# Performance work log

Measured on AMD Instinct MI355X. Metric: run time of the kernel, lower is better.

Reference implementation:

```python
import jax, jax.numpy as jnp
import numpy as np

D = 300   # hidden dim (Linear(300,300))
L = 160   # seq len, forced by W3 = Linear(160,1)


def _linear(x, W, b):
    # torch Linear: x @ W.T + b, W is (out, in)
    return jnp.matmul(x, W.T) + b


def setup_inputs() -> dict:
    key = jax.random.key(0)
    ks = jax.random.split(key, 16)
    B = 1024
    s = 1.0 / np.sqrt(D)
    inp = {
        'T_feature': jax.random.normal(ks[0], (B, L, D), jnp.float32),
        'CD_feature': jax.random.normal(ks[1], (B, L, D), jnp.float32),
        'Wproj': jax.random.normal(ks[2], (D, D), jnp.float32) * s,
        'bproj': jnp.zeros((D,), jnp.float32),
        'WqT_w': jax.random.normal(ks[3], (D, D), jnp.float32) * s,
        'WqT_b': jnp.zeros((D,), jnp.float32),
        'WqCD_w': jax.random.normal(ks[4], (D, D), jnp.float32) * s,
        'WqCD_b': jnp.zeros((D,), jnp.float32),
        'WkT_w': jax.random.normal(ks[5], (D, D), jnp.float32) * s,
        'WkT_b': jnp.zeros((D,), jnp.float32),
        'WkCD_w': jax.random.normal(ks[6], (D, D), jnp.float32) * s,
        'WkCD_b': jnp.zeros((D,), jnp.float32),
        'W3_w': jax.random.normal(ks[7], (1, L), jnp.float32) * (1.0 / np.sqrt(L)),
        'W3_b': jnp.zeros((1,), jnp.float32),
    }
    return inp


def reference(T_feature, CD_feature, Wproj, bproj, WqT_w, WqT_b, WqCD_w, WqCD_b,
              WkT_w, WkT_b, WkCD_w, WkCD_b, W3_w, W3_b):
    sqrt_d = jnp.sqrt(jnp.float32(D))
    proj_T = _linear(T_feature, Wproj, bproj)     # (B, L, D)
    proj_CD = _linear(CD_feature, Wproj, bproj)   # (B, L, D)

    # N_tensor @ proj_T is just the mean over tokens (weights 1/Len)
    mean_T = jnp.mean(proj_T, axis=1, keepdims=True)          # (B, 1, D)
    qT = _linear(mean_T, WqT_w, WqT_b)                        # (B, 1, D)
    kT = _linear(proj_T, WkT_w, WkT_b)                        # (B, L, D)
    alphaT = jnp.einsum('bqd,bkd->bqk', qT, kT) / sqrt_d      # (B, 1, L)
    ZT = jax.nn.sigmoid(alphaT)

    qCD = _linear(proj_CD, WqCD_w, WqCD_b)                    # (B, L, D)
    kCD = _linear(proj_CD, WkCD_w, WkCD_b)                    # (B, L, D)
    alphaCD = jnp.einsum('bqd,bkd->bqk', qCD, kCD) / sqrt_d   # (B, L, L)
    ZCD = jax.nn.sigmoid(alphaCD)

    # The per-token loop+cat is a plain broadcast multiply: Mt[:,i,:] = ZCD[:,i,:] * ZT[:,0,:]
    Mt = ZCD * ZT                                             # (B, L, L)
    alpha_f = jax.nn.softmax(_linear(Mt, W3_w, W3_b), axis=1) # (B, L, 1)

    # Second loop is a per-token scalar scale: HCD[:,i,:] = alpha_f[:,i,0] * proj_CD[:,i,:]
    HCD = alpha_f * proj_CD                                   # (B, L, D)
    return (proj_T, HCD)
```

## Files before the change

kernel.cpp:

```cpp
#include <hip/hip_runtime.h>
#include <hip/hip_bf16.h>


typedef __attribute__((ext_vector_type(8))) short short8;
typedef __attribute__((ext_vector_type(4))) float f32x4;

#define DP 320

__device__ __forceinline__ unsigned short f2bf(float x) {
  unsigned int u = __builtin_bit_cast(unsigned int, x);
  u += 0x7FFFu + ((u >> 16) & 1u);
  return (unsigned short)(u >> 16);
}
__device__ __forceinline__ float bf2f(unsigned short h) {
  unsigned int u = ((unsigned int)h) << 16;
  return __builtin_bit_cast(float, u);
}
__device__ __forceinline__ void gload16(const void* g, void* l) {
  __builtin_amdgcn_global_load_lds(
      (const __attribute__((address_space(1))) unsigned int*)g,
      (__attribute__((address_space(3))) unsigned int*)l, 16, 0, 0);
}
__device__ __forceinline__ float sigm(float x) { return 1.0f / (1.0f + __expf(-x)); }
__device__ __forceinline__ int swzc(int r, int c) {
  return (c & ~63) | ((((c >> 3) & 7) ^ (r & 7)) << 3) | (c & 7);
}

__global__ void wb_k(const float* __restrict__ W, unsigned short* __restrict__ Wb) {
  int n = blockIdx.x, c = threadIdx.x;
  unsigned short v = (n < 300 && c < 300) ? f2bf(W[n * 300 + c]) : (unsigned short)0;
  Wb[n * DP + swzc(n, c)] = v;
}

__global__ void crossdot_k(const float* __restrict__ Wa, const float* __restrict__ ba,
                           const float* __restrict__ Wc, const float* __restrict__ bc,
                           unsigned short* __restrict__ out_h, float* __restrict__ out_f,
                           float scale) {
  int n = blockIdx.x, c = threadIdx.x;
  float v = 0.f;
  if (n <= 300 && c <= 300) {
    for (int o = 0; o < 300; ++o) {
      float a = (c < 300) ? Wa[o * 300 + c] : ba[o];
      float b = (n < 300) ? Wc[o * 300 + n] : bc[o];
      v += a * b;
    }
    v *= scale;
  }
  if (out_h) out_h[n * DP + swzc(n, c)] = f2bf(v);
  else       out_f[n * DP + c] = v;
}

__global__ __launch_bounds__(256)
void cvt_k(const float* __restrict__ T, const float* __restrict__ CD,
           unsigned short* __restrict__ Abf) {
  unsigned idx = blockIdx.x * 256 + threadIdx.x;
  if (idx >= 327680u * 40u) return;
  unsigned row = idx / 40u, G = idx - row * 40u;
  int kc = G >> 3, sg = G & 7;
  int col0 = kc * 64 + (sg ^ ((int)row & 7)) * 8;
  const float* base = (row < 163840u) ? T + (size_t)row * 300
                                      : CD + (size_t)(row - 163840u) * 300;
  short8 h;
  if (col0 + 8 <= 300) {
    f32x4 x0 = *(const f32x4*)(base + col0), x1 = *(const f32x4*)(base + col0 + 4);
#pragma unroll
    for (int j = 0; j < 4; ++j) { h[j] = (short)f2bf(x0[j]); h[j + 4] = (short)f2bf(x1[j]); }
  } else {
#pragma unroll
    for (int j = 0; j < 8; ++j) {
      int c = col0 + j;
      h[j] = (short)((c < 300) ? f2bf(base[c]) : (unsigned short)0);
    }
  }
  *(short8*)(Abf + (size_t)row * DP + G * 8) = h;
}

__global__ __launch_bounds__(512)
void gemm_k(const unsigned short* __restrict__ Abf, const unsigned short* __restrict__ pCDg,
            const unsigned short* __restrict__ Wb, const unsigned short* __restrict__ Maug,
            const float* __restrict__ bias, float* __restrict__ Of,
            unsigned short* __restrict__ pCDout, unsigned short* __restrict__ Yout,
            int mode_base) {
  __shared__ __align__(16) unsigned short As[2][256 * 64];
  __shared__ __align__(16) unsigned short Bs[2][320 * 64];
  const int tid = threadIdx.x, wid = tid >> 6, lane = tid & 63;
  const int lr = lane & 15, hi = lane >> 4;
  const int mode = mode_base + blockIdx.y;
  const unsigned short* __restrict__ A =
      (mode == 0) ? Abf : (mode == 1) ? Abf + (size_t)163840 * DP : pCDg;
  const unsigned short* __restrict__ Bm = (mode == 2) ? Maug : Wb;
  const size_t m0 = (size_t)blockIdx.x * 256;

  f32x4 acc[4][10];
#pragma unroll
  for (int i = 0; i < 4; ++i)
#pragma unroll
    for (int j = 0; j < 10; ++j) acc[i][j] = (f32x4){0.f, 0.f, 0.f, 0.f};

  auto stageA = [&](int buf, int kc) {
#pragma unroll
    for (int it = 0; it < 4; ++it) {
      int idx = it * 512 + tid;
      int row = idx >> 3, g = idx & 7;
      gload16(A + (m0 + row) * DP + kc * 64 + g * 8, (char*)As[buf] + idx * 16);
    }
  };
  auto stageB = [&](int buf, int kc) {
#pragma unroll
    for (int it = 0; it < 5; ++it) {
      int idx = it * 512 + tid;
      int row = idx >> 3, g = idx & 7;
      gload16(Bm + (size_t)row * DP + kc * 64 + g * 8, (char*)Bs[buf] + idx * 16);
    }
  };

  stageA(0, 0); stageB(0, 0);
  __syncthreads();
  int buf = 0;
  const int rm = (wid >> 1) * 64, cn = (wid & 1) * 160;
  for (int kc = 0; kc < 5; ++kc) {
    if (kc < 4) { stageA(buf ^ 1, kc + 1); stageB(buf ^ 1, kc + 1); }
#pragma unroll
    for (int kk = 0; kk < 2; ++kk) {
      const int slot = ((kk * 4 + hi) ^ lr) & 7;
      short8 a[4];
#pragma unroll
      for (int mf = 0; mf < 4; ++mf)
        a[mf] = *(const short8*)((const char*)As[buf] + (rm + mf * 16 + lr) * 128 + slot * 16);
#pragma unroll
      for (int nh = 0; nh < 2; ++nh) {
        short8 b[5];
#pragma unroll
        for (int nf = 0; nf < 5; ++nf)
          b[nf] = *(const short8*)((const char*)Bs[buf] +
                                   (cn + (nh * 5 + nf) * 16 + lr) * 128 + slot * 16);
#pragma unroll
        for (int mf = 0; mf < 4; ++mf)
#pragma unroll
          for (int nf = 0; nf < 5; ++nf)
            acc[mf][nh * 5 + nf] =
                __builtin_amdgcn_mfma_f32_16x16x32_bf16(a[mf], b[nf], acc[mf][nh * 5 + nf], 0, 0, 0);
      }
    }
    __syncthreads();
    buf ^= 1;
  }

#pragma unroll
  for (int mf = 0; mf < 4; ++mf)
#pragma unroll
    for (int nf = 0; nf < 10; ++nf) {
      const int col = cn + nf * 16 + lr;
      const float bv = (mode < 2 && col < 300) ? bias[col] : 0.f;
#pragma unroll
      for (int r = 0; r < 4; ++r) {
        const size_t row = m0 + rm + mf * 16 + hi * 4 + r;
        float v = acc[mf][nf][r] + bv;
        if (mode == 0) {
          if (col < 300) Of[row * 300 + col] = v;
        } else {
          unsigned short u = (mode == 2) ? f2bf(v)
                           : (col < 300) ? f2bf(v)
                           : (col == 300) ? f2bf(1.0f) : (unsigned short)0;
          unsigned short* dst = (mode == 1) ? pCDout : Yout;
          dst[row * DP + swzc((int)row, col)] = u;
        }
      }
    }
}

__global__ __launch_bounds__(320)
void gate_k(const float* __restrict__ projT, const float* __restrict__ Pmat,
            float* __restrict__ ZT) {
  __shared__ float mt[304];
  __shared__ float vv[304];
  const int b = blockIdx.x, tid = threadIdx.x, wid = tid >> 6, lane = tid & 63;
  const float* p = projT + (size_t)b * 48000;
  if (tid < 300) {
    float s = 0.f;
#pragma unroll 4
    for (int l = 0; l < 160; ++l) s += p[l * 300 + tid];
    mt[tid] = s * (1.0f / 160.0f);
  }
  __syncthreads();
  if (tid <= 300) {
    float s = Pmat[300 * DP + tid];
    for (int a = 0; a < 300; ++a) s += Pmat[a * DP + tid] * mt[a];
    vv[tid] = s;
  }
  __syncthreads();
  for (int j = wid * 32; j < wid * 32 + 32; ++j) {
    const float* row = p + j * 300;
    float s = 0.f;
    for (int c = lane; c < 300; c += 64) s += vv[c] * row[c];
#pragma unroll
    for (int m = 1; m < 64; m <<= 1) s += __shfl_xor(s, m, 64);
    if (lane == 0) ZT[b * 160 + j] = sigm(s + vv[300]);
  }
}

__global__ __launch_bounds__(320)
void finale_k(const unsigned short* __restrict__ Yg, const unsigned short* __restrict__ Pg,
              const float* __restrict__ ZT, const float* __restrict__ W3w,
              float* __restrict__ out) {
  __shared__ __align__(16) unsigned short Ps[160 * DP];
  __shared__ __align__(16) unsigned short Ys[2][160 * 64];
  __shared__ float t_arr[160];
  __shared__ float s_arr[160];
  __shared__ float red0;
  const int b = blockIdx.x, tid = threadIdx.x, wid = tid >> 6, lane = tid & 63;
  const int lr = lane & 15, hi = lane >> 4;
  const unsigned short* Pb = Pg + (size_t)b * 160 * DP;
  const unsigned short* Yb = Yg + (size_t)b * 160 * DP;

  if (tid < 160) t_arr[tid] = ZT[b * 160 + tid] * W3w[tid];

#pragma unroll
  for (int it = 0; it < 20; ++it) {
    int idx = it * 320 + tid;
    gload16(Pb + (size_t)idx * 8, (char*)Ps + idx * 16);
  }
  auto stageY = [&](int buf, int kc) {
#pragma unroll
    for (int it = 0; it < 4; ++it) {
      int idx = it * 320 + tid;
      int row = idx >> 3, g = idx & 7;
      gload16(Yb + (size_t)row * DP + kc * 64 + g * 8, (char*)Ys[buf] + idx * 16);
    }
  };

  f32x4 acc[2][10];
#pragma unroll
  for (int i = 0; i < 2; ++i)
#pragma unroll
    for (int j = 0; j < 10; ++j) acc[i][j] = (f32x4){0.f, 0.f, 0.f, 0.f};

  stageY(0, 0);
  __syncthreads();
  int buf = 0;
  const int rm = wid * 32;
  for (int kc = 0; kc < 5; ++kc) {
    if (kc < 4) stageY(buf ^ 1, kc + 1);
#pragma unroll
    for (int kk = 0; kk < 2; ++kk) {
      const int slot = ((kk * 4 + hi) ^ lr) & 7;
      short8 a[2], bb[10];
#pragma unroll
      for (int mf = 0; mf < 2; ++mf)
        a[mf] = *(const short8*)((const char*)Ys[buf] + (rm + mf * 16 + lr) * 128 + slot * 16);
#pragma unroll
      for (int nf = 0; nf < 10; ++nf)
        bb[nf] = *(const short8*)((const char*)Ps + (nf * 16 + lr) * 640 + (kc * 8 + slot) * 16);
#pragma unroll
      for (int mf = 0; mf < 2; ++mf)
#pragma unroll
        for (int nf = 0; nf < 10; ++nf)
          acc[mf][nf] = __builtin_amdgcn_mfma_f32_16x16x32_bf16(a[mf], bb[nf], acc[mf][nf], 0, 0, 0);
    }
    __syncthreads();
    buf ^= 1;
  }

  float pp[2][4];
#pragma unroll
  for (int mf = 0; mf < 2; ++mf)
#pragma unroll
    for (int r = 0; r < 4; ++r) {
      float s = 0.f;
#pragma unroll
      for (int nf = 0; nf < 10; ++nf) s += sigm(acc[mf][nf][r]) * t_arr[nf * 16 + lr];
      pp[mf][r] = s;
    }
#pragma unroll
  for (int m = 1; m < 16; m <<= 1)
#pragma unroll
    for (int mf = 0; mf < 2; ++mf)
#pragma unroll
      for (int r = 0; r < 4; ++r) pp[mf][r] += __shfl_xor(pp[mf][r], m, 64);
  if (lr == 0) {
#pragma unroll
    for (int mf = 0; mf < 2; ++mf)
#pragma unroll
      for (int r = 0; r < 4; ++r)
        s_arr[rm + mf * 16 + hi * 4 + r] = pp[mf][r];
  }
  __syncthreads();
  if (wid == 0) {
    float v0 = s_arr[lane], v1 = s_arr[lane + 64];
    float v2 = (lane < 32) ? s_arr[lane + 128] : -3.0e38f;
    float mx = fmaxf(fmaxf(v0, v1), v2);
#pragma unroll
    for (int m = 1; m < 64; m <<= 1) mx = fmaxf(mx, __shfl_xor(mx, m, 64));
    float e0 = __expf(v0 - mx), e1 = __expf(v1 - mx);
    float e2 = (lane < 32) ? __expf(v2 - mx) : 0.f;
    s_arr[lane] = e0; s_arr[lane + 64] = e1;
    if (lane < 32) s_arr[lane + 128] = e2;
    float sm = e0 + e1 + e2;
#pragma unroll
    for (int m = 1; m < 64; m <<= 1) sm += __shfl_xor(sm, m, 64);
    if (lane == 0) red0 = 1.0f / sm;
  }
  __syncthreads();
  const float inv = red0;
  float* ob = out + (size_t)b * 48000;
#pragma unroll 2
  for (int it = 0; it < 19; ++it) {
    int idx = it * 320 + tid;
    if (idx < 6080) {
      int i = idx / 38, cg = idx - i * 38;
      int sg = (cg & ~7) | ((cg & 7) ^ (i & 7));
      short8 pv = *(const short8*)((const char*)Ps + i * 640 + sg * 16);
      float sc = s_arr[i] * inv;
      int c0 = cg * 8;
#pragma unroll
      for (int j = 0; j < 8; ++j) {
        int c = c0 + j;
        if (c < 300) ob[(size_t)i * 300 + c] = sc * bf2f((unsigned short)pv[j]);
      }
    }
  }
}

extern "C" void kernel_launch(void* const* d_in, const int* in_sizes, int n_in,
                              void* d_out, int out_size, void* d_ws, size_t ws_size,
                              hipStream_t stream) {
  (void)in_sizes; (void)n_in; (void)out_size; (void)ws_size;
  const float* T      = (const float*)d_in[0];
  const float* CD     = (const float*)d_in[1];
  const float* Wproj  = (const float*)d_in[2];
  const float* bproj  = (const float*)d_in[3];
  const float* WqT_w  = (const float*)d_in[4];
  const float* WqT_b  = (const float*)d_in[5];
  const float* WqCD_w = (const float*)d_in[6];
  const float* WqCD_b = (const float*)d_in[7];
  const float* WkT_w  = (const float*)d_in[8];
  const float* WkT_b  = (const float*)d_in[9];
  const float* WkCD_w = (const float*)d_in[10];
  const float* WkCD_b = (const float*)d_in[11];
  const float* W3_w   = (const float*)d_in[12];

  char* ws = (char*)d_ws;
  size_t off = 0;
  auto alloc = [&](size_t bytes) { void* p = ws + off; off = (off + bytes + 255) & ~(size_t)255; return p; };
  unsigned short* Abf   = (unsigned short*)alloc((size_t)327680 * DP * 2);
  unsigned short* Wb    = (unsigned short*)alloc((size_t)DP * DP * 2);
  unsigned short* MaugT = (unsigned short*)alloc((size_t)DP * DP * 2);
  float* Pmat = (float*)alloc((size_t)DP * DP * 4);
  float* ZT   = (float*)alloc((size_t)1024 * 160 * 4);

  float* projT = (float*)d_out;
  float* HCD   = (float*)d_out + (size_t)49152000;
  unsigned short* pCDg = Abf + (size_t)163840 * DP;
  unsigned short* Yg   = Abf;

  const float isd = 1.0f / sqrtf(300.0f);

  wb_k<<<dim3(320), dim3(320), 0, stream>>>(Wproj, Wb);
  crossdot_k<<<dim3(320), dim3(320), 0, stream>>>(WqCD_w, WqCD_b, WkCD_w, WkCD_b, MaugT, nullptr, isd);
  crossdot_k<<<dim3(320), dim3(320), 0, stream>>>(WkT_w, WkT_b, WqT_w, WqT_b, nullptr, Pmat, isd);
  cvt_k<<<dim3(51200), dim3(256), 0, stream>>>(T, CD, Abf);

  gemm_k<<<dim3(640, 2), dim3(512), 0, stream>>>(Abf, pCDg, Wb, MaugT, bproj,
                                                 projT, pCDg, Yg, 0);
  gate_k<<<dim3(1024), dim3(320), 0, stream>>>(projT, Pmat, ZT);
  gemm_k<<<dim3(640, 1), dim3(512), 0, stream>>>(Abf, pCDg, Wb, MaugT, bproj,
                                                 projT, pCDg, Yg, 2);
  finale_k<<<dim3(1024), dim3(320), 0, stream>>>(Yg, pCDg, ZT, W3_w, HCD);
}
```

Baseline: 775.5 us.

## Fold projection into attention weights so all three GEMMs run in one launch

Precomputes G = Maug·Wproj and a bias vector so the Y GEMM reads the raw bf16 CD input, not the projected pCD. This removes the dependency between the projection GEMM and the Y GEMM, so all three run as one gemm_k grid when the workspace is large enough for separate pCD and Y buffers. The gate kernel is rewritten to read the bf16 T input and fold Wproj into its vectors rather than reread the fp32 projT output. The cost is extra prep kernels and workspace, plus some accuracy risk because bf16 now feeds the gate path and the composed weight matrix is rounded to bf16.

```diff
diff --git a/kernel.cpp b/kernel.cpp
--- a/kernel.cpp
+++ b/kernel.cpp
@@ -26,28 +26,63 @@
   return (c & ~63) | ((((c >> 3) & 7) ^ (r & 7)) << 3) | (c & 7);
 }
 
-__global__ void wb_k(const float* __restrict__ W, unsigned short* __restrict__ Wb) {
-  int n = blockIdx.x, c = threadIdx.x;
-  unsigned short v = (n < 300 && c < 300) ? f2bf(W[n * 300 + c]) : (unsigned short)0;
-  Wb[n * DP + swzc(n, c)] = v;
-}
-
-__global__ void crossdot_k(const float* __restrict__ Wa, const float* __restrict__ ba,
-                           const float* __restrict__ Wc, const float* __restrict__ bc,
-                           unsigned short* __restrict__ out_h, float* __restrict__ out_f,
-                           float scale) {
-  int n = blockIdx.x, c = threadIdx.x;
+__global__ __launch_bounds__(320)
+void prep1_k(const float* __restrict__ W,
+             const float* __restrict__ WqCD_w, const float* __restrict__ WqCD_b,
+             const float* __restrict__ WkCD_w, const float* __restrict__ WkCD_b,
+             const float* __restrict__ WqT_w, const float* __restrict__ WqT_b,
+             const float* __restrict__ WkT_w, const float* __restrict__ WkT_b,
+             unsigned short* __restrict__ Wb, float* __restrict__ Wt,
+             unsigned short* __restrict__ MaugT, float* __restrict__ Maug_f,
+             float* __restrict__ Pmat, float isd) {
+  const int x = blockIdx.x, c = threadIdx.x;
+  if (x < 320) {
+    const int n = x;
+    unsigned short v = (n < 300 && c < 300) ? f2bf(W[n * 300 + c]) : (unsigned short)0;
+    Wb[n * DP + swzc(n, c)] = v;
+    if (n < 300 && c < 300) Wt[c * 304 + n] = W[n * 300 + c];
+  } else if (x < 640) {
+    const int n = x - 320;
+    float v = 0.f;
+    if (n <= 300 && c <= 300) {
+      for (int o = 0; o < 300; ++o) {
+        float a = (c < 300) ? WqCD_w[o * 300 + c] : WqCD_b[o];
+        float b = (n < 300) ? WkCD_w[o * 300 + n] : WkCD_b[o];
+        v += a * b;
+      }
+      v *= isd;
+    }
+    MaugT[n * DP + swzc(n, c)] = f2bf(v);
+    Maug_f[n * DP + c] = v;
+  } else {
+    const int n = x - 640;
+    float v = 0.f;
+    if (n <= 300 && c <= 300) {
+      for (int o = 0; o < 300; ++o) {
+        float a = (c < 300) ? WkT_w[o * 300 + c] : WkT_b[o];
+        float b = (n < 300) ? WqT_w[o * 300 + n] : WqT_b[o];
+        v += a * b;
+      }
+      v *= isd;
+    }
+    Pmat[n * DP + c] = v;
+  }
+}
+
+__global__ __launch_bounds__(320)
+void gh_k(const float* __restrict__ Maug_f, const float* __restrict__ W,
+          const float* __restrict__ bproj, unsigned short* __restrict__ Gswz,
+          float* __restrict__ h) {
+  const int n = blockIdx.x, o = threadIdx.x;
   float v = 0.f;
-  if (n <= 300 && c <= 300) {
-    for (int o = 0; o < 300; ++o) {
-      float a = (c < 300) ? Wa[o * 300 + c] : ba[o];
-      float b = (n < 300) ? Wc[o * 300 + n] : bc[o];
-      v += a * b;
-    }
-    v *= scale;
-  }
-  if (out_h) out_h[n * DP + swzc(n, c)] = f2bf(v);
-  else       out_f[n * DP + c] = v;
+  if (o < 300) {
+    for (int c = 0; c < 300; ++c) v += Maug_f[n * DP + c] * W[c * 300 + o];
+  } else if (o == 300) {
+    float s = 0.f;
+    for (int c = 0; c < 300; ++c) s += Maug_f[n * DP + c] * bproj[c];
+    h[n] = s + Maug_f[n * DP + 300];
+  }
+  Gswz[n * DP + swzc(n, o)] = (o < 300) ? f2bf(v) : (unsigned short)0;
 }
 
 __global__ __launch_bounds__(256)
@@ -57,7 +92,7 @@
   if (idx >= 327680u * 40u) return;
   unsigned row = idx / 40u, G = idx - row * 40u;
   int kc = G >> 3, sg = G & 7;
-  int col0 = kc * 64 + (sg ^ ((int)row & 7)) * 8;
+  int col0 = kc * 64 + ((sg ^ ((int)row & 7)) << 3);
   const float* base = (row < 163840u) ? T + (size_t)row * 300
                                       : CD + (size_t)(row - 163840u) * 300;
   short8 h;
@@ -76,19 +111,19 @@
 }
 
 __global__ __launch_bounds__(512)
-void gemm_k(const unsigned short* __restrict__ Abf, const unsigned short* __restrict__ pCDg,
-            const unsigned short* __restrict__ Wb, const unsigned short* __restrict__ Maug,
-            const float* __restrict__ bias, float* __restrict__ Of,
-            unsigned short* __restrict__ pCDout, unsigned short* __restrict__ Yout,
-            int mode_base) {
+void gemm_k(const unsigned short* __restrict__ A0, const unsigned short* __restrict__ A1,
+            const unsigned short* __restrict__ A2,
+            const unsigned short* __restrict__ B01, const unsigned short* __restrict__ B2,
+            const float* __restrict__ bias, const float* __restrict__ ybias,
+            float* __restrict__ Of, unsigned short* __restrict__ pCDout,
+            unsigned short* __restrict__ Yout, int mode_base) {
   __shared__ __align__(16) unsigned short As[2][256 * 64];
   __shared__ __align__(16) unsigned short Bs[2][320 * 64];
   const int tid = threadIdx.x, wid = tid >> 6, lane = tid & 63;
   const int lr = lane & 15, hi = lane >> 4;
   const int mode = mode_base + blockIdx.y;
-  const unsigned short* __restrict__ A =
-      (mode == 0) ? Abf : (mode == 1) ? Abf + (size_t)163840 * DP : pCDg;
-  const unsigned short* __restrict__ Bm = (mode == 2) ? Maug : Wb;
+  const unsigned short* __restrict__ A = (mode == 0) ? A0 : (mode == 1) ? A1 : A2;
+  const unsigned short* __restrict__ Bm = (mode == 2) ? B2 : B01;
   const size_t m0 = (size_t)blockIdx.x * 256;
 
   f32x4 acc[4][10];
@@ -151,7 +186,9 @@
 #pragma unroll
     for (int nf = 0; nf < 10; ++nf) {
       const int col = cn + nf * 16 + lr;
-      const float bv = (mode < 2 && col < 300) ? bias[col] : 0.f;
+      float bv;
+      if (mode == 2) bv = ybias ? ybias[col] : 0.f;
+      else bv = (col < 300) ? bias[col] : 0.f;
 #pragma unroll
       for (int r = 0; r < 4; ++r) {
         const size_t row = m0 + rm + mf * 16 + hi * 4 + r;
@@ -170,32 +207,78 @@
 }
 
 __global__ __launch_bounds__(320)
-void gate_k(const float* __restrict__ projT, const float* __restrict__ Pmat,
-            float* __restrict__ ZT) {
-  __shared__ float mt[304];
+void gate2_k(const unsigned short* __restrict__ AbfT, const float* __restrict__ Pmat,
+             const float* __restrict__ W, const float* __restrict__ Wt,
+             const float* __restrict__ bproj, float* __restrict__ ZT) {
+  __shared__ float part[8][320];
+  __shared__ float ml[320];
+  __shared__ float maug[304];
   __shared__ float vv[304];
-  const int b = blockIdx.x, tid = threadIdx.x, wid = tid >> 6, lane = tid & 63;
-  const float* p = projT + (size_t)b * 48000;
-  if (tid < 300) {
+  __shared__ float wt[320];
+  __shared__ float cpr;
+  const int b = blockIdx.x, t = threadIdx.x;
+  const int wid = t >> 6, lane = t & 63;
+  const size_t sbase = (size_t)b * 160 * DP;
+  {
+    const int og = t % 40, seg = t / 40;
+    float a8[8] = {0.f, 0.f, 0.f, 0.f, 0.f, 0.f, 0.f, 0.f};
+    for (int l = seg * 20; l < seg * 20 + 20; ++l) {
+      int sg = (og & ~7) | ((og & 7) ^ (l & 7));
+      short8 v = *(const short8*)(AbfT + sbase + (size_t)l * DP + sg * 8);
+#pragma unroll
+      for (int j = 0; j < 8; ++j) a8[j] += bf2f((unsigned short)v[j]);
+    }
+#pragma unroll
+    for (int j = 0; j < 8; ++j) part[seg][og * 8 + j] = a8[j];
+  }
+  __syncthreads();
+  {
     float s = 0.f;
-#pragma unroll 4
-    for (int l = 0; l < 160; ++l) s += p[l * 300 + tid];
-    mt[tid] = s * (1.0f / 160.0f);
-  }
-  __syncthreads();
-  if (tid <= 300) {
-    float s = Pmat[300 * DP + tid];
-    for (int a = 0; a < 300; ++a) s += Pmat[a * DP + tid] * mt[a];
-    vv[tid] = s;
+#pragma unroll
+    for (int sg = 0; sg < 8; ++sg) s += part[sg][t];
+    ml[t] = s * (1.0f / 160.0f);
+  }
+  __syncthreads();
+  if (t < 304) {
+    if (t < 300) {
+      float s = 0.f;
+      for (int o = 0; o < 300; ++o) s += Wt[o * 304 + t] * ml[o];
+      maug[t] = s + bproj[t];
+    } else maug[t] = (t == 300) ? 1.f : 0.f;
+  }
+  __syncthreads();
+  if (t < 304) {
+    float s = 0.f;
+    if (t <= 300) for (int a = 0; a <= 300; ++a) s += Pmat[a * DP + t] * maug[a];
+    vv[t] = s;
+  }
+  __syncthreads();
+  if (t < 320) {
+    if (t < 300) {
+      float s = 0.f;
+      for (int c = 0; c < 300; ++c) s += vv[c] * W[c * 300 + t];
+      wt[t] = s;
+    } else {
+      wt[t] = 0.f;
+      if (t == 300) {
+        float s = 0.f;
+        for (int c = 0; c < 300; ++c) s += vv[c] * bproj[c];
+        cpr = s + vv[300];
+      }
+    }
   }
   __syncthreads();
   for (int j = wid * 32; j < wid * 32 + 32; ++j) {
-    const float* row = p + j * 300;
     float s = 0.f;
-    for (int c = lane; c < 300; c += 64) s += vv[c] * row[c];
+    if (lane < 40) {
+      int sg = (lane & ~7) | ((lane & 7) ^ (j & 7));
+      short8 v = *(const short8*)(AbfT + sbase + (size_t)j * DP + sg * 8);
+#pragma unroll
+      for (int k = 0; k < 8; ++k) s += bf2f((unsigned short)v[k]) * wt[lane * 8 + k];
+    }
 #pragma unroll
     for (int m = 1; m < 64; m <<= 1) s += __shfl_xor(s, m, 64);
-    if (lane == 0) ZT[b * 160 + j] = sigm(s + vv[300]);
+    if (lane == 0) ZT[b * 160 + j] = sigm(s + cpr);
   }
 }
 
@@ -324,7 +407,7 @@
 extern "C" void kernel_launch(void* const* d_in, const int* in_sizes, int n_in,
                               void* d_out, int out_size, void* d_ws, size_t ws_size,
                               hipStream_t stream) {
-  (void)in_sizes; (void)n_in; (void)out_size; (void)ws_size;
+  (void)in_sizes; (void)n_in; (void)out_size;
   const float* T      = (const float*)d_in[0];
   const float* CD     = (const float*)d_in[1];
   const float* Wproj  = (const float*)d_in[2];
@@ -342,28 +425,45 @@
   char* ws = (char*)d_ws;
   size_t off = 0;
   auto alloc = [&](size_t bytes) { void* p = ws + off; off = (off + bytes + 255) & ~(size_t)255; return p; };
-  unsigned short* Abf   = (unsigned short*)alloc((size_t)327680 * DP * 2);
-  unsigned short* Wb    = (unsigned short*)alloc((size_t)DP * DP * 2);
-  unsigned short* MaugT = (unsigned short*)alloc((size_t)DP * DP * 2);
-  float* Pmat = (float*)alloc((size_t)DP * DP * 4);
-  float* ZT   = (float*)alloc((size_t)1024 * 160 * 4);
+  unsigned short* Wb     = (unsigned short*)alloc((size_t)DP * DP * 2);
+  unsigned short* MaugT  = (unsigned short*)alloc((size_t)DP * DP * 2);
+  unsigned short* Gswz   = (unsigned short*)alloc((size_t)DP * DP * 2);
+  float* Maug_f = (float*)alloc((size_t)DP * DP * 4);
+  float* Pmat   = (float*)alloc((size_t)DP * DP * 4);
+  float* Wt     = (float*)alloc((size_t)304 * 304 * 4);
+  float* hb     = (float*)alloc((size_t)DP * 4);
+  float* ZT     = (float*)alloc((size_t)1024 * 160 * 4);
+  unsigned short* Abf = (unsigned short*)alloc((size_t)327680 * DP * 2);
+  unsigned short* AbfCD = Abf + (size_t)163840 * DP;
+
+  const size_t half = (size_t)163840 * DP * 2;
+  const bool big = (ws_size > off) && ((ws_size - off) >= 2 * half + 1024);
+  unsigned short* pCDg = big ? (unsigned short*)alloc(half) : AbfCD;
+  unsigned short* Yg   = big ? (unsigned short*)alloc(half) : Abf;
 
   float* projT = (float*)d_out;
   float* HCD   = (float*)d_out + (size_t)49152000;
-  unsigned short* pCDg = Abf + (size_t)163840 * DP;
-  unsigned short* Yg   = Abf;
 
   const float isd = 1.0f / sqrtf(300.0f);
 
-  wb_k<<<dim3(320), dim3(320), 0, stream>>>(Wproj, Wb);
-  crossdot_k<<<dim3(320), dim3(320), 0, stream>>>(WqCD_w, WqCD_b, WkCD_w, WkCD_b, MaugT, nullptr, isd);
-  crossdot_k<<<dim3(320), dim3(320), 0, stream>>>(WkT_w, WkT_b, WqT_w, WqT_b, nullptr, Pmat, isd);
+  prep1_k<<<dim3(960), dim3(320), 0, stream>>>(Wproj, WqCD_w, WqCD_b, WkCD_w, WkCD_b,
+                                               WqT_w, WqT_b, WkT_w, WkT_b,
+                                               Wb, Wt, MaugT, Maug_f, Pmat, isd);
+  if (big)
+    gh_k<<<dim3(320), dim3(320), 0, stream>>>(Maug_f, Wproj, bproj, Gswz, hb);
   cvt_k<<<dim3(51200), dim3(256), 0, stream>>>(T, CD, Abf);
 
-  gemm_k<<<dim3(640, 2), dim3(512), 0, stream>>>(Abf, pCDg, Wb, MaugT, bproj,
-                                                 projT, pCDg, Yg, 0);
-  gate_k<<<dim3(1024), dim3(320), 0, stream>>>(projT, Pmat, ZT);
-  gemm_k<<<dim3(640, 1), dim3(512), 0, stream>>>(Abf, pCDg, Wb, MaugT, bproj,
-                                                 projT, pCDg, Yg, 2);
-  finale_k<<<dim3(1024), dim3(320), 0, stream>>>(Yg, pCDg, ZT, W3_w, HCD);
-}
+  if (big) {
+    gemm_k<<<dim3(640, 3), dim3(512), 0, stream>>>(Abf, AbfCD, AbfCD, Wb, Gswz,
+                                                   bproj, hb, projT, pCDg, Yg, 0);
+    gate2_k<<<dim3(1024), dim3(320), 0, stream>>>(Abf, Pmat, Wproj, Wt, bproj, ZT);
+    finale_k<<<dim3(1024), dim3(320), 0, stream>>>(Yg, pCDg, ZT, W3_w, HCD);
+  } else {
+    gemm_k<<<dim3(640, 2), dim3(512), 0, stream>>>(Abf, AbfCD, nullptr, Wb, nullptr,
+                                                   bproj, nullptr, projT, pCDg, nullptr, 0);
+    gate2_k<<<dim3(1024), dim3(320), 0, stream>>>(Abf, Pmat, Wproj, Wt, bproj, ZT);
+    gemm_k<<<dim3(640, 1), dim3(512), 0, stream>>>(Abf, AbfCD, pCDg, Wb, MaugT,
+                                                   bproj, nullptr, projT, pCDg, Yg, 2);
+    finale_k<<<dim3(1024), dim3(320), 0, stream>>>(Yg, pCDg, ZT, W3_w, HCD);
+  }
+}
```

Measured after the change: 731.1 us. 5.7% less time.
